# Performance work log

Measured on AMD Instinct MI355X. Metric: run time of the kernel, lower is better.

The kernel has to match this reference:

```python
import jax, jax.numpy as jnp
import numpy as np

N_NODES = 50000
N_EDGES = 800000
DIM = 128
HEADS = 2
DEPTH = 2
MLP = 512
NEG_SLOPE = 0.2  # PyG GATv2 default
EPS = 1e-5


def setup_inputs() -> dict:
    key = jax.random.key(0)
    ks = jax.random.split(key, 10)
    s = 0.05
    p = lambda k, shape: (jax.random.normal(k, shape, jnp.float32) * s)
    x = jax.random.normal(ks[0], (N_NODES, DIM), jnp.float32)
    edge_index = jax.random.randint(ks[1], (2, N_EDGES), 0, N_NODES, dtype=jnp.int64)
    D, H = DEPTH, HEADS
    return {
        "x": x,
        "edge_index": edge_index,
        # per-layer stacked params (leading dim = depth)
        "ln1_g": jnp.ones((D, DIM), jnp.float32), "ln1_b": jnp.zeros((D, DIM), jnp.float32),
        "Wl": p(ks[2], (D, DIM, H * DIM)), "bl": jnp.zeros((D, H * DIM), jnp.float32),
        "Wr": p(ks[3], (D, DIM, H * DIM)), "br": jnp.zeros((D, H * DIM), jnp.float32),
        "att": p(ks[4], (D, H, DIM)),
        "gat_b": jnp.zeros((D, H * DIM), jnp.float32),
        "proj_W": p(ks[5], (D, H * DIM, DIM)), "proj_b": jnp.zeros((D, DIM), jnp.float32),
        "ln2_g": jnp.ones((D, DIM), jnp.float32), "ln2_b": jnp.zeros((D, DIM), jnp.float32),
        "W1": p(ks[6], (D, DIM, MLP)), "b1": jnp.zeros((D, MLP), jnp.float32),
        "W2": p(ks[7], (D, MLP, DIM)), "b2": jnp.zeros((D, DIM), jnp.float32),
    }


def _layer_norm(x, g, b):
    m = jnp.mean(x, axis=-1, keepdims=True)
    v = jnp.var(x, axis=-1, keepdims=True)
    return (x - m) * jax.lax.rsqrt(v + EPS) * g + b


def _gatv2(x, src, dst, Wl, bl, Wr, br, att, gat_b):
    # GATv2Conv: e_ij = att^T LeakyReLU(Wl x_j + Wr x_i); alpha = segment-softmax over dst
    n = x.shape[0]
    xl = (x @ Wl + bl).reshape(n, HEADS, DIM)  # source transform [N,H,D]
    xr = (x @ Wr + br).reshape(n, HEADS, DIM)  # target transform [N,H,D]
    e = jax.nn.leaky_relu(xl[src] + xr[dst], NEG_SLOPE)      # [E,H,D]
    score = jnp.einsum('ehd,hd->eh', e, att)                 # [E,H]
    smax = jax.ops.segment_max(score, dst, num_segments=n)   # [N,H]
    ex = jnp.exp(score - smax[dst])
    denom = jax.ops.segment_sum(ex, dst, num_segments=n)     # [N,H]
    alpha = ex / (denom[dst] + 1e-16)                        # [E,H]
    msg = xl[src] * alpha[..., None]                         # [E,H,D]
    out = jax.ops.segment_sum(msg, dst, num_segments=n)      # [N,H,D]
    return out.reshape(n, HEADS * DIM) + gat_b


def reference(x, edge_index, ln1_g, ln1_b, Wl, bl, Wr, br, att, gat_b,
              proj_W, proj_b, ln2_g, ln2_b, W1, b1, W2, b2):
    src, dst = edge_index[0], edge_index[1]
    for i in range(DEPTH):
        h = _layer_norm(x, ln1_g[i], ln1_b[i])               # PreNorm
        g = _gatv2(h, src, dst, Wl[i], bl[i], Wr[i], br[i], att[i], gat_b[i])
        x = x + (g @ proj_W[i] + proj_b[i])                  # QuickFix proj + Residual
        h = _layer_norm(x, ln2_g[i], ln2_b[i])
        x = x + (jax.nn.gelu(h @ W1[i] + b1[i]) @ W2[i] + b2[i])  # FFN + Residual
    return x
```

## Files before the change

### kernel.cpp

```cpp
#include <hip/hip_runtime.h>

typedef unsigned int uint;
typedef unsigned short ushort;
typedef __attribute__((ext_vector_type(4))) float f32x4;
typedef __attribute__((ext_vector_type(2))) float f32x2;
typedef __attribute__((ext_vector_type(8))) short bf16x8;

#define N_NODES 50000
#define DIM 128
#define HEADS 2
#define HD 256
#define MLP 512
#define DEPTH 2
#define CAP 96

__device__ __forceinline__ uint f2bf(float f) {
    uint u = __float_as_uint(f);
    return (u + 0x7FFFu + ((u >> 16) & 1u)) >> 16;
}
__device__ __forceinline__ f32x2 bfpair(uint u) {
    f32x2 r;
    r.x = __uint_as_float(u << 16);
    r.y = __uint_as_float(u & 0xFFFF0000u);
    return r;
}

__device__ __forceinline__ float gelu_tanh(float x) {
    float t = 0.7978845608028654f * (x + 0.044715f * x * x * x);
    float e = __expf(2.0f * t);
    float th = 1.0f - 2.0f / (e + 1.0f);
    return 0.5f * x * (1.0f + th);
}

__global__ __launch_bounds__(256) void ln_kernel(
    const float* __restrict__ x, const float* __restrict__ g,
    const float* __restrict__ b, ushort* __restrict__ out, int N)
{
    int node = blockIdx.x * 4 + (threadIdx.x >> 6);
    if (node >= N) return;
    int lane = threadIdx.x & 63;
    const float2 v = *(const float2*)(x + (size_t)node * DIM + lane * 2);
    float s = v.x + v.y;
    float s2 = v.x * v.x + v.y * v.y;
    #pragma unroll
    for (int m = 1; m <= 32; m <<= 1) {
        s  += __shfl_xor(s,  m, 64);
        s2 += __shfl_xor(s2, m, 64);
    }
    float mean = s * (1.0f / 128.0f);
    float var  = s2 * (1.0f / 128.0f) - mean * mean;
    float rs = rsqrtf(var + 1e-5f);
    float ox = (v.x - mean) * rs * g[lane * 2]     + b[lane * 2];
    float oy = (v.y - mean) * rs * g[lane * 2 + 1] + b[lane * 2 + 1];
    uint pk = f2bf(ox) | (f2bf(oy) << 16);
    *(uint*)(out + (size_t)node * DIM + lane * 2) = pk;
}

__global__ __launch_bounds__(256) void wconv_all(
    const float* __restrict__ Wl, const float* __restrict__ Wr,
    const float* __restrict__ pW, const float* __restrict__ W1,
    const float* __restrict__ W2, ushort* __restrict__ WlWr_t,
    ushort* __restrict__ pW_t, ushort* __restrict__ W1_t,
    ushort* __restrict__ W2_t)
{
    int i = blockIdx.x * 256 + threadIdx.x;
    if (i < 65536) {
        int l = i >> 15, rem = i & 32767;
        int k = rem >> 8, m = rem & 255;
        WlWr_t[l * 65536 + m * 128 + k] = (ushort)f2bf(Wl[i]);
    } else if (i < 131072) {
        int j = i - 65536;
        int l = j >> 15, rem = j & 32767;
        int k = rem >> 8, m = rem & 255;
        WlWr_t[l * 65536 + (m + 256) * 128 + k] = (ushort)f2bf(Wr[j]);
    } else if (i < 196608) {
        int j = i - 131072;
        int l = j >> 15, rem = j & 32767;
        int k = rem >> 7, m = rem & 127;
        pW_t[l * 32768 + m * 256 + k] = (ushort)f2bf(pW[j]);
    } else if (i < 327680) {
        int j = i - 196608;
        int l = j >> 16, rem = j & 65535;
        int k = rem >> 9, m = rem & 511;
        W1_t[l * 65536 + m * 128 + k] = (ushort)f2bf(W1[j]);
    } else if (i < 458752) {
        int j = i - 327680;
        int l = j >> 16, rem = j & 65535;
        int k = rem >> 7, m = rem & 127;
        W2_t[l * 65536 + m * 512 + k] = (ushort)f2bf(W2[j]);
    }
}

template<int EPI>
__global__ __launch_bounds__(256) void gemm_mfma(
    const ushort* __restrict__ A, const ushort* __restrict__ Bt,
    const float* __restrict__ bias, const float* __restrict__ bias2, int bsplit,
    const float* __restrict__ R, void* __restrict__ Cout, int Nr, int K, int M)
{
    __shared__ ushort As[128 * 72];
    __shared__ ushort Bs[64 * 72];
    const int tid = threadIdx.x;
    const int wave = tid >> 6, lane = tid & 63;
    const int wm = wave >> 1, wn = wave & 1;
    const int r0 = blockIdx.y * 128;
    const int c0 = blockIdx.x * 64;
    const int l15 = lane & 15, q = lane >> 4;

    f32x4 acc[4][2];
    #pragma unroll
    for (int t = 0; t < 4; ++t)
        #pragma unroll
        for (int u = 0; u < 2; ++u) {
            f32x4 z = {0.f, 0.f, 0.f, 0.f};
            acc[t][u] = z;
        }

    for (int k0 = 0; k0 < K; k0 += 64) {
        #pragma unroll
        for (int p = 0; p < 4; ++p) {
            int flat = p * 256 + tid;
            int row = flat >> 3, c8 = flat & 7;
            int gr = r0 + row; gr = gr < Nr ? gr : Nr - 1;
            uint4 v = *(const uint4*)(A + (size_t)gr * K + k0 + c8 * 8);
            *(uint4*)(As + row * 72 + c8 * 8) = v;
        }
        #pragma unroll
        for (int p = 0; p < 2; ++p) {
            int flat = p * 256 + tid;
            int row = flat >> 3, c8 = flat & 7;
            uint4 v = *(const uint4*)(Bt + (size_t)(c0 + row) * K + k0 + c8 * 8);
            *(uint4*)(Bs + row * 72 + c8 * 8) = v;
        }
        __syncthreads();
        #pragma unroll
        for (int kh = 0; kh < 2; ++kh) {
            const int ko = kh * 32 + q * 8;
            bf16x8 a[4], b[2];
            #pragma unroll
            for (int t = 0; t < 4; ++t)
                a[t] = *(const bf16x8*)(As + (wm * 64 + t * 16 + l15) * 72 + ko);
            #pragma unroll
            for (int u = 0; u < 2; ++u)
                b[u] = *(const bf16x8*)(Bs + (wn * 32 + u * 16 + l15) * 72 + ko);
            #pragma unroll
            for (int t = 0; t < 4; ++t)
                #pragma unroll
                for (int u = 0; u < 2; ++u)
                    acc[t][u] = __builtin_amdgcn_mfma_f32_16x16x32_bf16(
                        a[t], b[u], acc[t][u], 0, 0, 0);
        }
        __syncthreads();
    }

    #pragma unroll
    for (int t = 0; t < 4; ++t) {
        int grow = r0 + wm * 64 + t * 16 + q * 4;
        #pragma unroll
        for (int u = 0; u < 2; ++u) {
            int gcol = c0 + wn * 32 + u * 16 + l15;
            float bv = (gcol < bsplit) ? bias[gcol] : bias2[gcol - bsplit];
            #pragma unroll
            for (int i = 0; i < 4; ++i) {
                int r = grow + i;
                if (r >= Nr) continue;
                float v = acc[t][u][i] + bv;
                if (EPI == 1) v = gelu_tanh(v);
                if (EPI == 2) {
                    v += R[(size_t)r * M + gcol];
                    ((float*)Cout)[(size_t)r * M + gcol] = v;
                } else {
                    ((ushort*)Cout)[(size_t)r * M + gcol] = (ushort)f2bf(v);
                }
            }
        }
    }
}

__global__ __launch_bounds__(256) void bucket_kernel(
    const int* __restrict__ src, const int* __restrict__ dst,
    int* __restrict__ deg, int* __restrict__ esrc, int E)
{
    int e = blockIdx.x * 256 + threadIdx.x;
    if (e >= E) return;
    int d = dst[e];
    int pos = atomicAdd(&deg[d], 1);
    if (pos < CAP) esrc[(size_t)d * CAP + pos] = src[e];
}

__global__ __launch_bounds__(256) void gat_gather(
    const int* __restrict__ deg, const int* __restrict__ esrc,
    const ushort* __restrict__ xlr, const float* __restrict__ att,
    const float* __restrict__ gat_b, ushort* __restrict__ agg, int N)
{
    int node = blockIdx.x * 4 + (threadIdx.x >> 6);
    if (node >= N) return;
    const int lane = threadIdx.x & 63;
    const int half = lane >> 5, sl = lane & 31;
    const int c = sl * 8;

    const uint4 rq = *(const uint4*)(xlr + (size_t)node * 512 + 256 + c);
    const f32x2 r01 = bfpair(rq.x), r23 = bfpair(rq.y);
    const f32x2 r45 = bfpair(rq.z), r67 = bfpair(rq.w);
    const float4 af0 = *(const float4*)(att + c);
    const float4 af1 = *(const float4*)(att + c + 4);
    const f32x2 a01 = {af0.x, af0.y}, a23 = {af0.z, af0.w};
    const f32x2 a45 = {af1.x, af1.y}, a67 = {af1.z, af1.w};

    int dc = deg[node]; dc = dc < CAP ? dc : CAP;
    const int base = node * CAP;
    f32x2 acc01 = {0.f, 0.f}, acc23 = {0.f, 0.f}, acc45 = {0.f, 0.f}, acc67 = {0.f, 0.f};
    float den = 0.f;

    if (dc > 0) {
        int slc = sl < dc ? sl : dc - 1;
        const int idxreg = esrc[base + slc];

        auto getsrc = [&](int e) -> int {
            int idx = e < dc ? e : dc - 1;
            int s = __shfl(idxreg, (lane & 32) | (idx & 31), 64);
            if (idx >= 32) s = esrc[base + idx];
            return s;
        };

        const int iters = (dc + 1) >> 1;
        int e0 = half;
        int s0 = getsrc(e0);
        uint4 lq0 = *(const uint4*)(xlr + (size_t)s0 * 512 + c);
        int e1 = e0 + 2;
        int s1 = getsrc(e1);
        uint4 lq1 = *(const uint4*)(xlr + (size_t)s1 * 512 + c);

        for (int it = 0; it < iters; ++it) {
            const int e2 = e0 + 4;
            const int s2 = getsrc(e2);
            const uint4 lq2 = *(const uint4*)(xlr + (size_t)s2 * 512 + c);

            const f32x2 l01 = bfpair(lq0.x), l23 = bfpair(lq0.y);
            const f32x2 l45 = bfpair(lq0.z), l67 = bfpair(lq0.w);
            f32x2 t, p2;
            t = l01 + r01; p2  = a01 * __builtin_elementwise_max(t, 0.2f * t);
            t = l23 + r23; p2 += a23 * __builtin_elementwise_max(t, 0.2f * t);
            t = l45 + r45; p2 += a45 * __builtin_elementwise_max(t, 0.2f * t);
            t = l67 + r67; p2 += a67 * __builtin_elementwise_max(t, 0.2f * t);
            float p = p2.x + p2.y;
            p += __shfl_xor(p, 1, 64);
            p += __shfl_xor(p, 2, 64);
            p += __shfl_xor(p, 4, 64);
            p += __shfl_xor(p, 8, 64);
            const float ex = (e0 < dc) ? __expf(p) : 0.f;
            acc01 += ex * l01; acc23 += ex * l23; acc45 += ex * l45; acc67 += ex * l67;
            den += ex;
            e0 = e1; lq0 = lq1;
            e1 = e2; lq1 = lq2;
        }
    }
    acc01.x += __shfl_xor(acc01.x, 32, 64); acc01.y += __shfl_xor(acc01.y, 32, 64);
    acc23.x += __shfl_xor(acc23.x, 32, 64); acc23.y += __shfl_xor(acc23.y, 32, 64);
    acc45.x += __shfl_xor(acc45.x, 32, 64); acc45.y += __shfl_xor(acc45.y, 32, 64);
    acc67.x += __shfl_xor(acc67.x, 32, 64); acc67.y += __shfl_xor(acc67.y, 32, 64);
    den     += __shfl_xor(den,     32, 64);

    if (half == 0) {
        const float inv = 1.0f / (den + 1e-16f);
        const float4 g0 = *(const float4*)(gat_b + c);
        const float4 g1 = *(const float4*)(gat_b + c + 4);
        uint4 o;
        o.x = f2bf(acc01.x * inv + g0.x) | (f2bf(acc01.y * inv + g0.y) << 16);
        o.y = f2bf(acc23.x * inv + g0.z) | (f2bf(acc23.y * inv + g0.w) << 16);
        o.z = f2bf(acc45.x * inv + g1.x) | (f2bf(acc45.y * inv + g1.y) << 16);
        o.w = f2bf(acc67.x * inv + g1.z) | (f2bf(acc67.y * inv + g1.w) << 16);
        *(uint4*)(agg + (size_t)node * HD + c) = o;
    }
}

extern "C" void kernel_launch(void* const* d_in, const int* in_sizes, int n_in,
                              void* d_out, int out_size, void* d_ws, size_t ws_size,
                              hipStream_t stream) {
    const float* x_in   = (const float*)d_in[0];
    const int*   eidx   = (const int*)d_in[1];
    const float* ln1_g  = (const float*)d_in[2];
    const float* ln1_b  = (const float*)d_in[3];
    const float* Wl     = (const float*)d_in[4];
    const float* bl     = (const float*)d_in[5];
    const float* Wr     = (const float*)d_in[6];
    const float* br     = (const float*)d_in[7];
    const float* att    = (const float*)d_in[8];
    const float* gat_b  = (const float*)d_in[9];
    const float* projW  = (const float*)d_in[10];
    const float* projb  = (const float*)d_in[11];
    const float* ln2_g  = (const float*)d_in[12];
    const float* ln2_b  = (const float*)d_in[13];
    const float* W1     = (const float*)d_in[14];
    const float* b1     = (const float*)d_in[15];
    const float* W2     = (const float*)d_in[16];
    const float* b2     = (const float*)d_in[17];

    const int N = N_NODES;
    const int E = in_sizes[1] / 2;
    const int* src = eidx;
    const int* dst = eidx + E;

    char* ws = (char*)d_ws;
    size_t off = 0;
    ushort* xlr  = (ushort*)(ws + off); off += (size_t)N * 512 * 2;
    ushort* agg  = (ushort*)(ws + off); off += (size_t)N * HD * 2;
    ushort* h    = (ushort*)(ws + off); off += (size_t)N * DIM * 2;
    ushort* WlWr_t = (ushort*)(ws + off); off += (size_t)DEPTH * 512 * 128 * 2;
    ushort* pW_t   = (ushort*)(ws + off); off += (size_t)DEPTH * 128 * 256 * 2;
    ushort* W1_t   = (ushort*)(ws + off); off += (size_t)DEPTH * 512 * 128 * 2;
    ushort* W2_t   = (ushort*)(ws + off); off += (size_t)DEPTH * 128 * 512 * 2;
    int* deg     = (int*)(ws + off);    off += (size_t)N * 4;
    int* esrc    = (int*)(ws + off);    off += (size_t)N * CAP * 4;
    ushort* mid  = xlr;

    float* x = (float*)d_out;

    const int nodeBlocks = (N + 3) / 4;
    const dim3 blk(256);
    const int gy = (N + 127) / 128;

    wconv_all<<<(458752 + 255) / 256, blk, 0, stream>>>(
        Wl, Wr, projW, W1, W2, WlWr_t, pW_t, W1_t, W2_t);

    hipMemsetAsync(deg, 0, (size_t)N * 4, stream);
    bucket_kernel<<<(E + 255) / 256, blk, 0, stream>>>(src, dst, deg, esrc, E);

    for (int L = 0; L < DEPTH; ++L) {
        const float* bl_i   = bl + (size_t)L * HD;
        const float* br_i   = br + (size_t)L * HD;
        const float* att_i  = att + (size_t)L * HD;
        const float* gatb_i = gat_b + (size_t)L * HD;
        const float* pb_i   = projb + (size_t)L * DIM;
        const float* b1_i   = b1 + (size_t)L * MLP;
        const float* b2_i   = b2 + (size_t)L * DIM;
        const float* xin_L  = (L == 0) ? x_in : x;

        ln_kernel<<<nodeBlocks, blk, 0, stream>>>(xin_L, ln1_g + L * DIM, ln1_b + L * DIM, h, N);
        gemm_mfma<0><<<dim3(8, gy), blk, 0, stream>>>(
            h, WlWr_t + (size_t)L * 512 * 128, bl_i, br_i, HD, nullptr, xlr, N, 128, 512);
        gat_gather<<<nodeBlocks, blk, 0, stream>>>(deg, esrc, xlr, att_i, gatb_i, agg, N);
        gemm_mfma<2><<<dim3(2, gy), blk, 0, stream>>>(
            agg, pW_t + (size_t)L * 128 * 256, pb_i, pb_i, 1 << 30, xin_L, x, N, 256, 128);
        ln_kernel<<<nodeBlocks, blk, 0, stream>>>(x, ln2_g + L * DIM, ln2_b + L * DIM, h, N);
        gemm_mfma<1><<<dim3(8, gy), blk, 0, stream>>>(
            h, W1_t + (size_t)L * 512 * 128, b1_i, b1_i, 1 << 30, nullptr, mid, N, 128, 512);
        gemm_mfma<2><<<dim3(2, gy), blk, 0, stream>>>(
            mid, W2_t + (size_t)L * 128 * 512, b2_i, b2_i, 1 << 30, x, x, N, 512, 128);
    }
}
```

Baseline: 556.3 us.

## Fuse projection GEMM with residual and LayerNorm; merge weight conversion with edge bucketing

Adds a proj_ln kernel in which each 64-row block computes the full 128-wide projection output, adds bias and residual, writes x, and computes LayerNorm across waves through shared memory to emit bf16 h directly. This removes the separate ln_kernel launch and its re-read of x. Weight conversion and edge bucketing are also merged into one prep kernel to save a launch. In exchange the projection GEMM uses smaller row tiles over the full width, which may change occupancy and reuse of the weight tile.

```diff
diff --git a/kernel.cpp b/kernel.cpp
--- a/kernel.cpp
+++ b/kernel.cpp
@@ -56,12 +56,14 @@
     *(uint*)(out + (size_t)node * DIM + lane * 2) = pk;
 }
 
-__global__ __launch_bounds__(256) void wconv_all(
+__global__ __launch_bounds__(256) void prep_kernel(
     const float* __restrict__ Wl, const float* __restrict__ Wr,
     const float* __restrict__ pW, const float* __restrict__ W1,
     const float* __restrict__ W2, ushort* __restrict__ WlWr_t,
     ushort* __restrict__ pW_t, ushort* __restrict__ W1_t,
-    ushort* __restrict__ W2_t)
+    ushort* __restrict__ W2_t,
+    const int* __restrict__ src, const int* __restrict__ dst,
+    int* __restrict__ deg, int* __restrict__ esrc, int E)
 {
     int i = blockIdx.x * 256 + threadIdx.x;
     if (i < 65536) {
@@ -88,6 +90,13 @@
         int l = j >> 16, rem = j & 65535;
         int k = rem >> 7, m = rem & 127;
         W2_t[l * 65536 + m * 512 + k] = (ushort)f2bf(W2[j]);
+    } else {
+        int e = i - 458752;
+        if (e < E) {
+            int d = dst[e];
+            int pos = atomicAdd(&deg[d], 1);
+            if (pos < CAP) esrc[(size_t)d * CAP + pos] = src[e];
+        }
     }
 }
 
@@ -176,15 +185,134 @@
     }
 }
 
-__global__ __launch_bounds__(256) void bucket_kernel(
-    const int* __restrict__ src, const int* __restrict__ dst,
-    int* __restrict__ deg, int* __restrict__ esrc, int E)
+__global__ __launch_bounds__(256) void proj_ln(
+    const ushort* __restrict__ A, const ushort* __restrict__ Bt,
+    const float* __restrict__ pb, const float* __restrict__ xin,
+    const float* __restrict__ lng, const float* __restrict__ lnb,
+    float* __restrict__ x, ushort* __restrict__ h, int Nr)
 {
-    int e = blockIdx.x * 256 + threadIdx.x;
-    if (e >= E) return;
-    int d = dst[e];
-    int pos = atomicAdd(&deg[d], 1);
-    if (pos < CAP) esrc[(size_t)d * CAP + pos] = src[e];
+    __shared__ ushort As[64 * 72];
+    __shared__ ushort Bs[128 * 72];
+    __shared__ float red[64][4];
+    const int tid = threadIdx.x;
+    const int wave = tid >> 6, lane = tid & 63;
+    const int wm = wave >> 1, wn = wave & 1;
+    const int r0 = blockIdx.y * 64;
+    const int l15 = lane & 15, q = lane >> 4;
+    const int K = 256;
+
+    f32x4 acc[2][4];
+    #pragma unroll
+    for (int t = 0; t < 2; ++t)
+        #pragma unroll
+        for (int u = 0; u < 4; ++u) {
+            f32x4 z = {0.f, 0.f, 0.f, 0.f};
+            acc[t][u] = z;
+        }
+
+    for (int k0 = 0; k0 < K; k0 += 64) {
+        #pragma unroll
+        for (int p = 0; p < 2; ++p) {
+            int flat = p * 256 + tid;
+            int row = flat >> 3, c8 = flat & 7;
+            int gr = r0 + row; gr = gr < Nr ? gr : Nr - 1;
+            uint4 v = *(const uint4*)(A + (size_t)gr * K + k0 + c8 * 8);
+            *(uint4*)(As + row * 72 + c8 * 8) = v;
+        }
+        #pragma unroll
+        for (int p = 0; p < 4; ++p) {
+            int flat = p * 256 + tid;
+            int row = flat >> 3, c8 = flat & 7;
+            uint4 v = *(const uint4*)(Bt + (size_t)row * K + k0 + c8 * 8);
+            *(uint4*)(Bs + row * 72 + c8 * 8) = v;
+        }
+        __syncthreads();
+        #pragma unroll
+        for (int kh = 0; kh < 2; ++kh) {
+            const int ko = kh * 32 + q * 8;
+            bf16x8 a[2], b[4];
+            #pragma unroll
+            for (int t = 0; t < 2; ++t)
+                a[t] = *(const bf16x8*)(As + (wm * 32 + t * 16 + l15) * 72 + ko);
+            #pragma unroll
+            for (int u = 0; u < 4; ++u)
+                b[u] = *(const bf16x8*)(Bs + (wn * 64 + u * 16 + l15) * 72 + ko);
+            #pragma unroll
+            for (int t = 0; t < 2; ++t)
+                #pragma unroll
+                for (int u = 0; u < 4; ++u)
+                    acc[t][u] = __builtin_amdgcn_mfma_f32_16x16x32_bf16(
+                        a[t], b[u], acc[t][u], 0, 0, 0);
+        }
+        __syncthreads();
+    }
+
+    float vreg[2][4][4];
+    float s[2][4], s2[2][4];
+    #pragma unroll
+    for (int t = 0; t < 2; ++t)
+        #pragma unroll
+        for (int i = 0; i < 4; ++i) { s[t][i] = 0.f; s2[t][i] = 0.f; }
+
+    #pragma unroll
+    for (int t = 0; t < 2; ++t) {
+        #pragma unroll
+        for (int u = 0; u < 4; ++u) {
+            int gcol = wn * 64 + u * 16 + l15;
+            float bv = pb[gcol];
+            #pragma unroll
+            for (int i = 0; i < 4; ++i) {
+                int r = r0 + wm * 32 + t * 16 + q * 4 + i;
+                int rc = r < Nr ? r : Nr - 1;
+                float v = acc[t][u][i] + bv + xin[(size_t)rc * DIM + gcol];
+                if (r < Nr) x[(size_t)r * DIM + gcol] = v;
+                vreg[t][u][i] = v;
+                s[t][i]  += v;
+                s2[t][i] += v * v;
+            }
+        }
+    }
+    #pragma unroll
+    for (int t = 0; t < 2; ++t)
+        #pragma unroll
+        for (int i = 0; i < 4; ++i) {
+            #pragma unroll
+            for (int m = 1; m <= 8; m <<= 1) {
+                s[t][i]  += __shfl_xor(s[t][i],  m, 64);
+                s2[t][i] += __shfl_xor(s2[t][i], m, 64);
+            }
+        }
+    if (l15 == 0) {
+        #pragma unroll
+        for (int t = 0; t < 2; ++t)
+            #pragma unroll
+            for (int i = 0; i < 4; ++i) {
+                int row = wm * 32 + t * 16 + q * 4 + i;
+                red[row][wn * 2]     = s[t][i];
+                red[row][wn * 2 + 1] = s2[t][i];
+            }
+    }
+    __syncthreads();
+    #pragma unroll
+    for (int t = 0; t < 2; ++t) {
+        #pragma unroll
+        for (int i = 0; i < 4; ++i) {
+            int row = wm * 32 + t * 16 + q * 4 + i;
+            float S  = red[row][0] + red[row][2];
+            float S2 = red[row][1] + red[row][3];
+            float mean = S * (1.0f / 128.0f);
+            float var  = S2 * (1.0f / 128.0f) - mean * mean;
+            float rs = rsqrtf(var + 1e-5f);
+            int r = r0 + row;
+            if (r >= Nr) continue;
+            #pragma unroll
+            for (int u = 0; u < 4; ++u) {
+                int gcol = wn * 64 + u * 16 + l15;
+                float hv = (vreg[t][u][i] - mean) * rs * lng[gcol] + lnb[gcol];
+                h[(size_t)r * DIM + gcol] = (ushort)f2bf(hv);
+            }
+        }
+    }
 }
 
 __global__ __launch_bounds__(256) void gat_gather(
@@ -318,12 +446,15 @@
     const int nodeBlocks = (N + 3) / 4;
     const dim3 blk(256);
     const int gy = (N + 127) / 128;
-
-    wconv_all<<<(458752 + 255) / 256, blk, 0, stream>>>(
-        Wl, Wr, projW, W1, W2, WlWr_t, pW_t, W1_t, W2_t);
+    const int gy64 = (N + 63) / 64;
 
     hipMemsetAsync(deg, 0, (size_t)N * 4, stream);
-    bucket_kernel<<<(E + 255) / 256, blk, 0, stream>>>(src, dst, deg, esrc, E);
+    {
+        int total = 458752 + E;
+        prep_kernel<<<(total + 255) / 256, blk, 0, stream>>>(
+            Wl, Wr, projW, W1, W2, WlWr_t, pW_t, W1_t, W2_t,
+            src, dst, deg, esrc, E);
+    }
 
     for (int L = 0; L < DEPTH; ++L) {
         const float* bl_i   = bl + (size_t)L * HD;
@@ -339,9 +470,9 @@
         gemm_mfma<0><<<dim3(8, gy), blk, 0, stream>>>(
             h, WlWr_t + (size_t)L * 512 * 128, bl_i, br_i, HD, nullptr, xlr, N, 128, 512);
         gat_gather<<<nodeBlocks, blk, 0, stream>>>(deg, esrc, xlr, att_i, gatb_i, agg, N);
-        gemm_mfma<2><<<dim3(2, gy), blk, 0, stream>>>(
-            agg, pW_t + (size_t)L * 128 * 256, pb_i, pb_i, 1 << 30, xin_L, x, N, 256, 128);
-        ln_kernel<<<nodeBlocks, blk, 0, stream>>>(x, ln2_g + L * DIM, ln2_b + L * DIM, h, N);
+        proj_ln<<<dim3(1, gy64), blk, 0, stream>>>(
+            agg, pW_t + (size_t)L * 128 * 256, pb_i, xin_L,
+            ln2_g + L * DIM, ln2_b + L * DIM, x, h, N);
         gemm_mfma<1><<<dim3(8, gy), blk, 0, stream>>>(
             h, W1_t + (size_t)L * 512 * 128, b1_i, b1_i, 1 << 30, nullptr, mid, N, 128, 512);
         gemm_mfma<2><<<dim3(2, gy), blk, 0, stream>>>(
```

Measured after the change: 568.3 us. 2.2% more time.
